# Kernel optimization log

Measured on AMD Instinct MI355X. Metric: run time of the kernel, lower is better.

Reference implementation:

```python
import jax, jax.numpy as jnp
import numpy as np

EPS = 1e-6

def act_quant(x):
    # per-token int8 absmax quantization with straight-through estimator
    scale = 127.0 / jnp.clip(jnp.max(jnp.abs(x), axis=-1, keepdims=True), 1e-5)
    q = jnp.clip(jnp.round(x * scale), -128.0, 127.0) / scale
    return x + jax.lax.stop_gradient(q - x)

def weight_quant(w):
    # ternary absmean quantization with straight-through estimator
    scale = 1.0 / jnp.clip(jnp.mean(jnp.abs(w)), 1e-5)
    q = jnp.clip(jnp.round(w * scale), -1.0, 1.0) / scale
    return w + jax.lax.stop_gradient(q - w)

def bit_linear(x, w):
    # x: [..., in], w: [out, in]
    return jnp.einsum('...i,oi->...o', act_quant(x), weight_quant(w))

def subln(x, g):
    # RMSNorm over last dim with learnable gain
    var = jnp.mean(jnp.square(x), axis=-1, keepdims=True)
    return x * jax.lax.rsqrt(var + EPS) * g

def setup_inputs() -> dict:
    key = jax.random.key(0)
    k1, k2, k3 = jax.random.split(key, 3)
    B, S, H, I = 8, 8192, 512, 2048
    x = jax.random.normal(k1, (B, S, H), dtype=jnp.float32)
    w_up = jax.random.normal(k2, (I, H), dtype=jnp.float32) * (H ** -0.5)
    w_down = jax.random.normal(k3, (H, I), dtype=jnp.float32) * (I ** -0.5)
    g = jnp.ones((I,), dtype=jnp.float32)
    return {'x': x, 'w_up': w_up, 'w_down': w_down, 'g': g}

def reference(x, w_up, w_down, g):
    h = bit_linear(x, w_up)            # [B,S,I]
    h = jnp.square(jax.nn.relu(h))     # relu^2 activation
    h = subln(h, g)                    # SubLN (RMSNorm)
    return bit_linear(h, w_down)       # [B,S,H]
```

## Files before the change

### kernel.cpp

```cpp
#include <hip/hip_runtime.h>
#include <stdint.h>


typedef int v4i __attribute__((ext_vector_type(4)));

#define AS1(p) ((const __attribute__((address_space(1))) void*)(p))
#define AS3(p) ((__attribute__((address_space(3))) void*)(p))

static constexpr int CHUNK = 32768;
static constexpr size_t OFF_PART = 256;
static constexpr size_t OFF_SX   = 8192;
static constexpr size_t OFF_INV2 = OFF_SX   + 262144;
static constexpr size_t OFF_WUQ  = OFF_INV2 + 262144;
static constexpr size_t OFF_WDQ  = OFF_WUQ  + 1048576;
static constexpr size_t OFF_XQ   = OFF_WDQ  + 1048576;
static constexpr size_t OFF_Z16  = OFF_XQ   + 33554432;
static constexpr size_t OFF_HQ   = OFF_Z16  + 134217728;

__global__ void wabs_partial(const float* __restrict__ w, double* __restrict__ part)
{
    int t = threadIdx.x, bid = blockIdx.x;
    const float4* w4 = (const float4*)w;
    int base = bid * 256 + t;
    double s = 0.0;
    #pragma unroll
    for (int j = 0; j < 4; ++j) {
        float4 v = w4[base + j * 65536];
        s += (double)fabsf(v.x) + (double)fabsf(v.y)
           + (double)fabsf(v.z) + (double)fabsf(v.w);
    }
    #pragma unroll
    for (int off = 32; off > 0; off >>= 1) s += __shfl_down(s, off);
    __shared__ double ps[4];
    int l = t & 63, wv = t >> 6;
    if (l == 0) ps[wv] = s;
    __syncthreads();
    if (t == 0) part[bid] = ((ps[0] + ps[1]) + ps[2]) + ps[3];
}

__global__ void finalize_sums(const double* __restrict__ part, double* __restrict__ sums)
{
    int t = threadIdx.x;
    double a = part[t];
    double b = part[256 + t];
    #pragma unroll
    for (int off = 32; off > 0; off >>= 1) {
        a += __shfl_down(a, off);
        b += __shfl_down(b, off);
    }
    __shared__ double pa[4], pb[4];
    int l = t & 63, wv = t >> 6;
    if (l == 0) { pa[wv] = a; pb[wv] = b; }
    __syncthreads();
    if (t == 0) {
        sums[0] = ((pa[0] + pa[1]) + pa[2]) + pa[3];
        sums[1] = ((pb[0] + pb[1]) + pb[2]) + pb[3];
    }
}

__global__ void wquant(const float* __restrict__ w, const double* __restrict__ sum,
                       signed char* __restrict__ wq)
{
    int i = blockIdx.x * blockDim.x + threadIdx.x;
    if (i >= 262144) return;
    float mean  = (float)(*sum) * (1.0f / 1048576.0f);
    float scale = 1.0f / fmaxf(mean, 1e-5f);
    float4 v = ((const float4*)w)[i];
    int q0 = (int)fminf(fmaxf(rintf(v.x * scale), -1.f), 1.f);
    int q1 = (int)fminf(fmaxf(rintf(v.y * scale), -1.f), 1.f);
    int q2 = (int)fminf(fmaxf(rintf(v.z * scale), -1.f), 1.f);
    int q3 = (int)fminf(fmaxf(rintf(v.w * scale), -1.f), 1.f);
    unsigned pk = (q0 & 255) | ((q1 & 255) << 8) | ((q2 & 255) << 16) | ((q3 & 255) << 24);
    ((unsigned*)wq)[i] = pk;
}

__global__ void xquant(const float* __restrict__ x, signed char* __restrict__ xq,
                       float* __restrict__ inv_sx)
{
    int row = blockIdx.x * 4 + (threadIdx.x >> 6);
    int l   = threadIdx.x & 63;
    const float* xr = x + (size_t)row * 512;
    float4 v0 = *(const float4*)(xr + l * 8);
    float4 v1 = *(const float4*)(xr + l * 8 + 4);
    float m = fmaxf(fmaxf(fmaxf(fabsf(v0.x), fabsf(v0.y)), fmaxf(fabsf(v0.z), fabsf(v0.w))),
                    fmaxf(fmaxf(fabsf(v1.x), fabsf(v1.y)), fmaxf(fabsf(v1.z), fabsf(v1.w))));
    #pragma unroll
    for (int off = 1; off < 64; off <<= 1) m = fmaxf(m, __shfl_xor(m, off));
    float mc = fmaxf(m, 1e-5f);
    float s  = 127.0f / mc;
    int q[8];
    q[0] = (int)fminf(fmaxf(rintf(v0.x * s), -128.f), 127.f);
    q[1] = (int)fminf(fmaxf(rintf(v0.y * s), -128.f), 127.f);
    q[2] = (int)fminf(fmaxf(rintf(v0.z * s), -128.f), 127.f);
    q[3] = (int)fminf(fmaxf(rintf(v0.w * s), -128.f), 127.f);
    q[4] = (int)fminf(fmaxf(rintf(v1.x * s), -128.f), 127.f);
    q[5] = (int)fminf(fmaxf(rintf(v1.y * s), -128.f), 127.f);
    q[6] = (int)fminf(fmaxf(rintf(v1.z * s), -128.f), 127.f);
    q[7] = (int)fminf(fmaxf(rintf(v1.w * s), -128.f), 127.f);
    uint2 pk;
    pk.x = (q[0] & 255) | ((q[1] & 255) << 8) | ((q[2] & 255) << 16) | ((q[3] & 255) << 24);
    pk.y = (q[4] & 255) | ((q[5] & 255) << 8) | ((q[6] & 255) << 16) | ((q[7] & 255) << 24);
    *(uint2*)(xq + (size_t)row * 512 + l * 8) = pk;
    if (l == 0) inv_sx[row] = mc * (1.0f / 127.0f);
}

__global__ __launch_bounds__(256)
void norm_quant(const short* __restrict__ z16, const float* __restrict__ inv_sx,
                const double* __restrict__ wsum, const float* __restrict__ g,
                signed char* __restrict__ hq, float* __restrict__ inv2)
{
    int row = blockIdx.x;
    int t = threadIdx.x;
    float wmean = fmaxf((float)wsum[0] * (1.0f / 1048576.0f), 1e-5f);
    float f = inv_sx[row] * wmean;

    v4i zi = *(const v4i*)(z16 + (size_t)row * 2048 + t * 8);
    const short* zs = (const short*)&zi;
    float4 g0 = *(const float4*)(g + t * 8);
    float4 g1 = *(const float4*)(g + t * 8 + 4);
    float gv[8] = {g0.x, g0.y, g0.z, g0.w, g1.x, g1.y, g1.z, g1.w};

    float h[8];
    float ss = 0.f, mm = 0.f;
    #pragma unroll
    for (int j = 0; j < 8; ++j) {
        float z = (float)zs[j] * f;
        float a = fmaxf(z, 0.f);
        h[j] = a * a;
        ss += h[j] * h[j];
        mm  = fmaxf(mm, fabsf(h[j] * gv[j]));
    }
    #pragma unroll
    for (int off = 1; off < 64; off <<= 1) {
        ss += __shfl_xor(ss, off);
        mm  = fmaxf(mm, __shfl_xor(mm, off));
    }
    __shared__ float sss[4], smm[4];
    int l = t & 63, wv = t >> 6;
    if (l == 0) { sss[wv] = ss; smm[wv] = mm; }
    __syncthreads();
    float sst = ((sss[0] + sss[1]) + sss[2]) + sss[3];
    float mmt = fmaxf(fmaxf(smm[0], smm[1]), fmaxf(smm[2], smm[3]));

    float var  = sst * (1.0f / 2048.0f);
    float r    = 1.0f / sqrtf(var + 1e-6f);
    float maxy = fmaxf(r * mmt, 1e-5f);
    float sc   = 127.0f / maxy;
    if (t == 0) inv2[row] = maxy * (1.0f / 127.0f);

    int q[8];
    #pragma unroll
    for (int j = 0; j < 8; ++j) {
        float y = (h[j] * r) * gv[j];
        q[j] = (int)fminf(fmaxf(rintf(y * sc), -128.f), 127.f);
    }
    uint2 pk;
    pk.x = (q[0] & 255) | ((q[1] & 255) << 8) | ((q[2] & 255) << 16) | ((q[3] & 255) << 24);
    pk.y = (q[4] & 255) | ((q[5] & 255) << 8) | ((q[6] & 255) << 16) | ((q[7] & 255) << 24);
    *(uint2*)(hq + (size_t)row * 2048 + t * 8) = pk;
}

template<int K, int N, int EPI>
__global__ __launch_bounds__(256, 4)
void gemm_i8(const signed char* __restrict__ A,
             const signed char* __restrict__ B,
             const float* __restrict__ rowscale,
             const double* __restrict__ wsum,
             short* __restrict__ z16,
             float* __restrict__ out)
{
    constexpr int NKT = K / 64;
    constexpr int NBN = N / 128;
    __shared__ __align__(16) char smem[32768];

    int nwg  = gridDim.x;
    int orig = blockIdx.x;
    int q8 = nwg >> 3, r8 = nwg & 7;
    int xcd = orig & 7, lin = orig >> 3;
    int swz = (xcd < r8 ? xcd * (q8 + 1) : r8 * (q8 + 1) + (xcd - r8) * q8) + lin;
    int mt = swz / NBN, nt = swz - mt * NBN;

    size_t mbase = (size_t)mt * 128;
    int    nbase = nt * 128;

    int t = threadIdx.x;
    int l = t & 63;
    int wid = t >> 6;
    int wr = wid >> 1, wc = wid & 1;

    v4i acc[4][4] = {};

    const signed char* Ab = A + mbase * K;
    const signed char* Bb = B + (size_t)nbase * K;

    auto stage = [&](int p, int kt) {
        char* lA = smem + p * 16384;
        char* lB = lA + 8192;
        int k0 = kt * 64;
        #pragma unroll
        for (int i = 0; i < 2; ++i) {
            int lin16 = i * 256 + t;
            int row   = lin16 >> 2;
            int c     = (lin16 & 3) ^ ((row >> 1) & 3);
            __builtin_amdgcn_global_load_lds(AS1(Ab + (size_t)row * K + k0 + c * 16),
                                             AS3(lA + lin16 * 16), 16, 0, 0);
            __builtin_amdgcn_global_load_lds(AS1(Bb + (size_t)row * K + k0 + c * 16),
                                             AS3(lB + lin16 * 16), 16, 0, 0);
        }
    };

    stage(0, 0);
    __syncthreads();

    for (int kt = 0; kt < NKT; ++kt) {
        int p = kt & 1;
        if (kt + 1 < NKT) stage(p ^ 1, kt + 1);
        const char* lA = smem + p * 16384;
        const char* lB = lA + 8192;
        v4i af[4], bf[4];
        #pragma unroll
        for (int r = 0; r < 4; ++r) {
            int arow = wr * 64 + r * 16 + (l & 15);
            int ac   = (l >> 4) ^ ((arow >> 1) & 3);
            af[r] = *reinterpret_cast<const v4i*>(lA + (arow * 4 + ac) * 16);
            int brow = wc * 64 + r * 16 + (l & 15);
            int bc   = (l >> 4) ^ ((brow >> 1) & 3);
            bf[r] = *reinterpret_cast<const v4i*>(lB + (brow * 4 + bc) * 16);
        }
        #pragma unroll
        for (int r = 0; r < 4; ++r)
            #pragma unroll
            for (int c = 0; c < 4; ++c)
                acc[r][c] = __builtin_amdgcn_mfma_i32_16x16x64_i8(af[r], bf[c], acc[r][c], 0, 0, 0);
        __syncthreads();
    }

    int rsub = wr * 64 + 4 * (l >> 4);
    int csub = wc * 64 + (l & 15);

    if constexpr (EPI == 0) {
        short* sm = (short*)smem;
        #pragma unroll
        for (int rt = 0; rt < 4; ++rt)
            #pragma unroll
            for (int reg = 0; reg < 4; ++reg) {
                int rho = rsub + rt * 16 + reg;
                #pragma unroll
                for (int ct = 0; ct < 4; ++ct)
                    sm[rho * 128 + csub + ct * 16] = (short)acc[rt][ct][reg];
            }
        __syncthreads();
        #pragma unroll
        for (int it = 0; it < 8; ++it) {
            int j = it * 256 + t;
            int rho = j >> 4, ck = j & 15;
            *(v4i*)(z16 + (size_t)(mbase + rho) * 2048 + nbase + ck * 8) =
                *(const v4i*)(sm + rho * 128 + ck * 8);
        }
    } else {
        float wmean = fmaxf((float)wsum[0] * (1.0f / 1048576.0f), 1e-5f);
        #pragma unroll
        for (int rt = 0; rt < 4; ++rt)
            #pragma unroll
            for (int reg = 0; reg < 4; ++reg) {
                size_t grow = mbase + rsub + rt * 16 + reg;
                float f = rowscale[grow] * wmean;
                #pragma unroll
                for (int ct = 0; ct < 4; ++ct)
                    out[grow * N + nbase + csub + ct * 16] = (float)acc[rt][ct][reg] * f;
            }
    }
}

extern "C" void kernel_launch(void* const* d_in, const int* in_sizes, int n_in,
                              void* d_out, int out_size, void* d_ws, size_t ws_size,
                              hipStream_t stream)
{
    const float* x  = (const float*)d_in[0];
    const float* wu = (const float*)d_in[1];
    const float* wd = (const float*)d_in[2];
    const float* g  = (const float*)d_in[3];
    float* out = (float*)d_out;
    char*  ws  = (char*)d_ws;

    double* sums     = (double*)ws;
    double* part     = (double*)(ws + OFF_PART);
    float*  inv_sx   = (float*)(ws + OFF_SX);
    float*  inv2     = (float*)(ws + OFF_INV2);
    signed char* wuq = (signed char*)(ws + OFF_WUQ);
    signed char* wdq = (signed char*)(ws + OFF_WDQ);
    signed char* xq  = (signed char*)(ws + OFF_XQ);
    short*  z16      = (short*)(ws + OFF_Z16);
    signed char* hq  = (signed char*)(ws + OFF_HQ);

    wabs_partial<<<256, 256, 0, stream>>>(wu, part);
    wabs_partial<<<256, 256, 0, stream>>>(wd, part + 256);
    finalize_sums<<<1, 256, 0, stream>>>(part, sums);
    wquant<<<1024, 256, 0, stream>>>(wu, sums + 0, wuq);
    wquant<<<1024, 256, 0, stream>>>(wd, sums + 1, wdq);
    xquant<<<16384, 256, 0, stream>>>(x, xq, inv_sx);

    for (int c = 0; c < 2; ++c) {
        size_t R = (size_t)c * CHUNK;
        gemm_i8<512, 2048, 0><<<(CHUNK / 128) * 16, 256, 0, stream>>>(
            xq + R * 512, wuq, nullptr, nullptr, z16, nullptr);
        norm_quant<<<CHUNK, 256, 0, stream>>>(z16, inv_sx + R, sums + 0, g,
                                              hq, inv2 + R);
        gemm_i8<2048, 512, 2><<<(CHUNK / 128) * 4, 256, 0, stream>>>(
            hq, wdq, inv2 + R, sums + 1, nullptr, out + R * 512);
    }
}
```

Baseline: 505.6 us.

## Drop token chunking, merge weight kernels, use wave-per-row norm_quant

Removes the two-chunk loop so each GEMM and the norm/quant kernel runs once over all 65536 tokens, with the z16 workspace doubled to hold the full intermediate. The weight abs-sum and ternary quant kernels for both matrices are merged into single launches. norm_quant now gives each row to one 64-lane wave, so the block-level shared-memory reduction and barrier go away. The aim is fewer launches and larger grids per kernel, at the cost of a bigger intermediate buffer whose write and re-read may fall out of cache, and more registers per thread in norm_quant.

```diff
diff --git a/kernel.cpp b/kernel.cpp
--- a/kernel.cpp
+++ b/kernel.cpp
@@ -7,7 +7,7 @@
 #define AS1(p) ((const __attribute__((address_space(1))) void*)(p))
 #define AS3(p) ((__attribute__((address_space(3))) void*)(p))
 
-static constexpr int CHUNK = 32768;
+static constexpr int MTOK = 65536;
 static constexpr size_t OFF_PART = 256;
 static constexpr size_t OFF_SX   = 8192;
 static constexpr size_t OFF_INV2 = OFF_SX   + 262144;
@@ -15,13 +15,15 @@
 static constexpr size_t OFF_WDQ  = OFF_WUQ  + 1048576;
 static constexpr size_t OFF_XQ   = OFF_WDQ  + 1048576;
 static constexpr size_t OFF_Z16  = OFF_XQ   + 33554432;
-static constexpr size_t OFF_HQ   = OFF_Z16  + 134217728;
-
-__global__ void wabs_partial(const float* __restrict__ w, double* __restrict__ part)
+static constexpr size_t OFF_HQ   = OFF_Z16  + 268435456;
+
+__global__ void wabs_partial2(const float* __restrict__ wu,
+                              const float* __restrict__ wd,
+                              double* __restrict__ part)
 {
     int t = threadIdx.x, bid = blockIdx.x;
-    const float4* w4 = (const float4*)w;
-    int base = bid * 256 + t;
+    const float4* w4 = (const float4*)(bid < 256 ? wu : wd);
+    int base = (bid & 255) * 256 + t;
     double s = 0.0;
     #pragma unroll
     for (int j = 0; j < 4; ++j) {
@@ -58,20 +60,23 @@
     }
 }
 
-__global__ void wquant(const float* __restrict__ w, const double* __restrict__ sum,
-                       signed char* __restrict__ wq)
+__global__ void wquant2(const float* __restrict__ wu, const float* __restrict__ wd,
+                        const double* __restrict__ sums,
+                        signed char* __restrict__ wuq, signed char* __restrict__ wdq)
 {
     int i = blockIdx.x * blockDim.x + threadIdx.x;
-    if (i >= 262144) return;
-    float mean  = (float)(*sum) * (1.0f / 1048576.0f);
+    bool up = i < 262144;
+    int j = up ? i : i - 262144;
+    const float4* w = (const float4*)(up ? wu : wd);
+    unsigned* dst   = (unsigned*)(up ? wuq : wdq);
+    float mean  = (float)(up ? sums[0] : sums[1]) * (1.0f / 1048576.0f);
     float scale = 1.0f / fmaxf(mean, 1e-5f);
-    float4 v = ((const float4*)w)[i];
+    float4 v = w[j];
     int q0 = (int)fminf(fmaxf(rintf(v.x * scale), -1.f), 1.f);
     int q1 = (int)fminf(fmaxf(rintf(v.y * scale), -1.f), 1.f);
     int q2 = (int)fminf(fmaxf(rintf(v.z * scale), -1.f), 1.f);
     int q3 = (int)fminf(fmaxf(rintf(v.w * scale), -1.f), 1.f);
-    unsigned pk = (q0 & 255) | ((q1 & 255) << 8) | ((q2 & 255) << 16) | ((q3 & 255) << 24);
-    ((unsigned*)wq)[i] = pk;
+    dst[j] = (q0 & 255) | ((q1 & 255) << 8) | ((q2 & 255) << 16) | ((q3 & 255) << 24);
 }
 
 __global__ void xquant(const float* __restrict__ x, signed char* __restrict__ xq,
@@ -109,55 +114,57 @@
                 const double* __restrict__ wsum, const float* __restrict__ g,
                 signed char* __restrict__ hq, float* __restrict__ inv2)
 {
-    int row = blockIdx.x;
-    int t = threadIdx.x;
+    int row = blockIdx.x * 4 + (threadIdx.x >> 6);
+    int l   = threadIdx.x & 63;
     float wmean = fmaxf((float)wsum[0] * (1.0f / 1048576.0f), 1e-5f);
     float f = inv_sx[row] * wmean;
 
-    v4i zi = *(const v4i*)(z16 + (size_t)row * 2048 + t * 8);
-    const short* zs = (const short*)&zi;
-    float4 g0 = *(const float4*)(g + t * 8);
-    float4 g1 = *(const float4*)(g + t * 8 + 4);
-    float gv[8] = {g0.x, g0.y, g0.z, g0.w, g1.x, g1.y, g1.z, g1.w};
-
-    float h[8];
+    const short* zr = z16 + (size_t)row * 2048;
+    float hg[32];
     float ss = 0.f, mm = 0.f;
     #pragma unroll
-    for (int j = 0; j < 8; ++j) {
-        float z = (float)zs[j] * f;
-        float a = fmaxf(z, 0.f);
-        h[j] = a * a;
-        ss += h[j] * h[j];
-        mm  = fmaxf(mm, fabsf(h[j] * gv[j]));
+    for (int j = 0; j < 4; ++j) {
+        int cols = j * 512 + l * 8;
+        v4i zi = *(const v4i*)(zr + cols);
+        const short* zs = (const short*)&zi;
+        float4 g0 = *(const float4*)(g + cols);
+        float4 g1 = *(const float4*)(g + cols + 4);
+        float gv[8] = {g0.x, g0.y, g0.z, g0.w, g1.x, g1.y, g1.z, g1.w};
+        #pragma unroll
+        for (int e = 0; e < 8; ++e) {
+            float z = (float)zs[e] * f;
+            float a = fmaxf(z, 0.f);
+            float h = a * a;
+            ss += h * h;
+            float y = h * gv[e];
+            hg[j * 8 + e] = y;
+            mm = fmaxf(mm, fabsf(y));
+        }
     }
     #pragma unroll
     for (int off = 1; off < 64; off <<= 1) {
         ss += __shfl_xor(ss, off);
         mm  = fmaxf(mm, __shfl_xor(mm, off));
     }
-    __shared__ float sss[4], smm[4];
-    int l = t & 63, wv = t >> 6;
-    if (l == 0) { sss[wv] = ss; smm[wv] = mm; }
-    __syncthreads();
-    float sst = ((sss[0] + sss[1]) + sss[2]) + sss[3];
-    float mmt = fmaxf(fmaxf(smm[0], smm[1]), fmaxf(smm[2], smm[3]));
-
-    float var  = sst * (1.0f / 2048.0f);
+    float var  = ss * (1.0f / 2048.0f);
     float r    = 1.0f / sqrtf(var + 1e-6f);
-    float maxy = fmaxf(r * mmt, 1e-5f);
+    float maxy = fmaxf(r * mm, 1e-5f);
     float sc   = 127.0f / maxy;
-    if (t == 0) inv2[row] = maxy * (1.0f / 127.0f);
-
-    int q[8];
-    #pragma unroll
-    for (int j = 0; j < 8; ++j) {
-        float y = (h[j] * r) * gv[j];
-        q[j] = (int)fminf(fmaxf(rintf(y * sc), -128.f), 127.f);
-    }
-    uint2 pk;
-    pk.x = (q[0] & 255) | ((q[1] & 255) << 8) | ((q[2] & 255) << 16) | ((q[3] & 255) << 24);
-    pk.y = (q[4] & 255) | ((q[5] & 255) << 8) | ((q[6] & 255) << 16) | ((q[7] & 255) << 24);
-    *(uint2*)(hq + (size_t)row * 2048 + t * 8) = pk;
+    if (l == 0) inv2[row] = maxy * (1.0f / 127.0f);
+
+    #pragma unroll
+    for (int j = 0; j < 4; ++j) {
+        int q[8];
+        #pragma unroll
+        for (int e = 0; e < 8; ++e) {
+            float y = hg[j * 8 + e] * r;
+            q[e] = (int)fminf(fmaxf(rintf(y * sc), -128.f), 127.f);
+        }
+        uint2 pk;
+        pk.x = (q[0] & 255) | ((q[1] & 255) << 8) | ((q[2] & 255) << 16) | ((q[3] & 255) << 24);
+        pk.y = (q[4] & 255) | ((q[5] & 255) << 8) | ((q[6] & 255) << 16) | ((q[7] & 255) << 24);
+        *(uint2*)(hq + (size_t)row * 2048 + j * 512 + l * 8) = pk;
+    }
 }
 
 template<int K, int N, int EPI>
@@ -293,20 +300,14 @@
     short*  z16      = (short*)(ws + OFF_Z16);
     signed char* hq  = (signed char*)(ws + OFF_HQ);
 
-    wabs_partial<<<256, 256, 0, stream>>>(wu, part);
-    wabs_partial<<<256, 256, 0, stream>>>(wd, part + 256);
+    wabs_partial2<<<512, 256, 0, stream>>>(wu, wd, part);
     finalize_sums<<<1, 256, 0, stream>>>(part, sums);
-    wquant<<<1024, 256, 0, stream>>>(wu, sums + 0, wuq);
-    wquant<<<1024, 256, 0, stream>>>(wd, sums + 1, wdq);
+    wquant2<<<2048, 256, 0, stream>>>(wu, wd, sums, wuq, wdq);
     xquant<<<16384, 256, 0, stream>>>(x, xq, inv_sx);
 
-    for (int c = 0; c < 2; ++c) {
-        size_t R = (size_t)c * CHUNK;
-        gemm_i8<512, 2048, 0><<<(CHUNK / 128) * 16, 256, 0, stream>>>(
-            xq + R * 512, wuq, nullptr, nullptr, z16, nullptr);
-        norm_quant<<<CHUNK, 256, 0, stream>>>(z16, inv_sx + R, sums + 0, g,
-                                              hq, inv2 + R);
-        gemm_i8<2048, 512, 2><<<(CHUNK / 128) * 4, 256, 0, stream>>>(
-            hq, wdq, inv2 + R, sums + 1, nullptr, out + R * 512);
-    }
-}
+    gemm_i8<512, 2048, 0><<<(MTOK / 128) * 16, 256, 0, stream>>>(
+        xq, wuq, nullptr, nullptr, z16, nullptr);
+    norm_quant<<<MTOK / 4, 256, 0, stream>>>(z16, inv_sx, sums, g, hq, inv2);
+    gemm_i8<2048, 512, 2><<<(MTOK / 128) * 4, 256, 0, stream>>>(
+        hq, wdq, inv2, sums + 1, nullptr, out);
+}
```

After: 512.1 us. About the same (+1.3%).
